# Performance work log

Measured on AMD Instinct MI355X. Metric: run time of the kernel, lower is better.

The kernel has to match this reference:

```python
import jax, jax.numpy as jnp
import numpy as np

WZ, WH, WW = 2, 6, 12            # window_size (pressure, lat, lon)
DIM, HEADS = 192, 6
N_TOK = WZ * WH * WW             # 144 tokens per window
TYPE_WIN = (14 // WZ) * (721 // WH)  # 840 window types
TABLE = (2 * WW - 1) * WH * WH * WZ * WZ  # 3312 bias rows


def _position_index():
    # Earth-specific (asymmetric in z/h) relative position index, per _construct_index
    zi = np.arange(WZ); zj = -np.arange(WZ) * WZ
    hi = np.arange(WH); hj = -np.arange(WH) * WH
    w = np.arange(WW)
    c1 = np.stack(np.meshgrid(zi, hi, w, indexing='ij')).reshape(3, -1)
    c2 = np.stack(np.meshgrid(zj, hj, w, indexing='ij')).reshape(3, -1)
    coords = (c1[:, :, None] - c2[:, None, :]).transpose(1, 2, 0)
    coords[:, :, 2] += WW - 1
    coords[:, :, 1] *= 2 * WW - 1
    coords[:, :, 0] *= (2 * WW - 1) * WH * WH
    return jnp.asarray(coords.sum(-1).reshape(-1), dtype=jnp.int32)  # (N*N,)


def setup_inputs() -> dict:
    key = jax.random.key(0)
    ks = jax.random.split(key, 8)
    B = 2
    x = jax.random.normal(ks[0], (B, TYPE_WIN, N_TOK, DIM), dtype=jnp.float32)
    mask = jax.random.normal(ks[1], (B, N_TOK, N_TOK), dtype=jnp.float32)
    w1 = jax.random.normal(ks[2], (3 * DIM, DIM), dtype=jnp.float32) * 0.02
    b1 = jnp.zeros((3 * DIM,), dtype=jnp.float32)
    w2 = jax.random.normal(ks[3], (DIM, DIM), dtype=jnp.float32) * 0.02
    b2 = jnp.zeros((DIM,), dtype=jnp.float32)
    bias_table = jax.random.normal(ks[4], (TABLE, TYPE_WIN, HEADS), dtype=jnp.float32) * 0.02
    return {"x": x, "mask": mask, "w1": w1, "b1": b1, "w2": w2, "b2": b2,
            "bias_table": bias_table, "position_index": _position_index()}


def reference(x, mask, w1, b1, w2, b2, bias_table, position_index):
    B, nW, N, C = x.shape
    d = C // HEADS
    scale = d ** (-0.5)
    qkv = (jnp.einsum('bwnc,oc->bwno', x, w1) + b1).reshape(B, nW, N, 3, HEADS, d)
    q, k, v = jnp.moveaxis(qkv, 3, 0)           # each (B, nW, N, H, d)
    attn = jnp.einsum('bwnhd,bwmhd->bwhnm', q * scale, k)  # (B, nW, H, N, N)
    # gather earth-specific bias: (N*N,) -> (N, N, nW, H) -> (nW, H, N, N)
    bias = bias_table[position_index].reshape(N, N, nW, HEADS).transpose(2, 3, 0, 1)
    attn = attn + bias[None] + mask[:, None, None, :, :]
    attn = jax.nn.softmax(attn, axis=-1)
    out = jnp.einsum('bwhnm,bwmhd->bwnhd', attn, v).reshape(B, nW, N, C)
    return jnp.einsum('bwnc,oc->bwno', out, w2) + b2
```

## Files before the change

### kernel.cpp

```cpp
#include <hip/hip_runtime.h>
#include <cstdint>
#include <cstddef>

typedef unsigned short u16;
typedef __bf16 bf16x8 __attribute__((ext_vector_type(8)));
typedef u16    u16x8  __attribute__((ext_vector_type(8)));
typedef float  f32x4  __attribute__((ext_vector_type(4)));

#define NW 840
#define NTOK 144
#define DIM 192
#define HEADS 6
#define TABLE_ROWS 3312
#define SCALE 0.17677669529663687f

__device__ __forceinline__ u16 f2b_bits(float f) {
  unsigned u = __builtin_bit_cast(unsigned, f);
  return (u16)((u + 0x7FFFu + ((u >> 16) & 1u)) >> 16);
}

__device__ __forceinline__ bf16x8 ld_bf8(const u16* p) {
  return __builtin_bit_cast(bf16x8, *(const u16x8*)p);
}

__device__ __forceinline__ f32x4 mfma16(bf16x8 a, bf16x8 b, f32x4 c) {
  return __builtin_amdgcn_mfma_f32_16x16x32_bf16(a, b, c, 0, 0, 0);
}

__global__ void k_prep(const float* __restrict__ bt, const float* __restrict__ w1,
                       const float* __restrict__ w2, float* __restrict__ bto,
                       u16* __restrict__ w1b, u16* __restrict__ w2b) {
  __shared__ float tile[64 * 65];
  int bid = blockIdx.x, tid = threadIdx.x;
  if (bid < 52 * 79) {
    int p0 = (bid % 52) * 64;
    int wh0 = (bid / 52) * 64;
    #pragma unroll
    for (int it = 0; it < 16; ++it) {
      int idx = tid + it * 256;
      int pp = idx >> 6, cc = idx & 63;
      float v = 0.f;
      if (p0 + pp < TABLE_ROWS && wh0 + cc < NW * HEADS)
        v = bt[(size_t)(p0 + pp) * (NW * HEADS) + wh0 + cc];
      tile[pp * 65 + cc] = v;
    }
    __syncthreads();
    #pragma unroll
    for (int it = 0; it < 16; ++it) {
      int idx = tid + it * 256;
      int rr = idx >> 6, cc2 = idx & 63;
      if (wh0 + rr < NW * HEADS && p0 + cc2 < TABLE_ROWS)
        bto[(size_t)(wh0 + rr) * TABLE_ROWS + p0 + cc2] = tile[cc2 * 65 + rr];
    }
  } else {
    int i = (bid - 52 * 79) * 256 + tid;
    if (i < 576 * DIM) {
      w1b[i] = f2b_bits(w1[i]);
    } else {
      int j = i - 576 * DIM;
      if (j < DIM * DIM) w2b[j] = f2b_bits(w2[j]);
    }
  }
}

__global__ __launch_bounds__(576) void k_attn(
    const float* __restrict__ x, const float* __restrict__ mask,
    const float* __restrict__ b1, const u16* __restrict__ w1b,
    const float* __restrict__ bias_t, const int* __restrict__ pos,
    u16* __restrict__ Ow) {
  __shared__ __align__(16) u16 q_lds[NTOK * 40];
  __shared__ __align__(16) u16 k_lds[NTOK * 40];
  __shared__ __align__(16) u16 vt[32 * 168];
  __shared__ __align__(16) u16 pch[NTOK * 40];
  __shared__ float bias_s[TABLE_ROWS];

  const int tid = threadIdx.x;
  const int w = tid >> 6;
  const int l = tid & 63;
  const int c = l & 15;
  const int q4 = l >> 4;
  const int bw = blockIdx.x;
  const int b = bw / NW;
  const int ww = bw % NW;

  const float* xg = x + (size_t)bw * (NTOK * DIM);

  if (tid < 512) vt[(tid >> 4) * 168 + 144 + (tid & 15)] = 0;

  const int m3 = w % 3;
  const int p = w / 3;
  const int r = w;
  bf16x8 xf[3][6];
  #pragma unroll
  for (int i = 0; i < 3; ++i) {
    const int mti = m3 + 3 * i;
    const float* rp = xg + (size_t)(mti * 16 + c) * DIM;
    #pragma unroll
    for (int ks = 0; ks < 6; ++ks) {
      const float4* fp = (const float4*)(rp + ks * 32 + q4 * 8);
      float4 f0 = fp[0], f1 = fp[1];
      u16x8 rr;
      rr[0] = f2b_bits(f0.x); rr[1] = f2b_bits(f0.y);
      rr[2] = f2b_bits(f0.z); rr[3] = f2b_bits(f0.w);
      rr[4] = f2b_bits(f1.x); rr[5] = f2b_bits(f1.y);
      rr[6] = f2b_bits(f1.z); rr[7] = f2b_bits(f1.w);
      xf[i][ks] = __builtin_bit_cast(bf16x8, rr);
    }
  }

  const f32x4 z = {0.f, 0.f, 0.f, 0.f};
  const int n0 = r * 16 + q4 * 4;
  const int* pr[4];
  const float* mr[4];
  #pragma unroll
  for (int g = 0; g < 4; ++g) {
    pr[g] = pos + (n0 + g) * NTOK;
    mr[g] = mask + (size_t)b * (NTOK * NTOK) + (size_t)(n0 + g) * NTOK;
  }

  for (int h = 0; h < HEADS; ++h) {
    f32x4 acc[3][2];
    #pragma unroll
    for (int i = 0; i < 3; ++i) { acc[i][0] = z; acc[i][1] = z; }
    const int obase = p * DIM + h * 32;
    #pragma unroll
    for (int ks = 0; ks < 6; ++ks) {
      bf16x8 w0 = ld_bf8(w1b + (size_t)(obase + c) * DIM + ks * 32 + q4 * 8);
      bf16x8 w1f = ld_bf8(w1b + (size_t)(obase + 16 + c) * DIM + ks * 32 + q4 * 8);
      #pragma unroll
      for (int i = 0; i < 3; ++i) {
        acc[i][0] = mfma16(xf[i][ks], w0, acc[i][0]);
        acc[i][1] = mfma16(xf[i][ks], w1f, acc[i][1]);
      }
    }
    float b1v[2] = {b1[obase + c], b1[obase + 16 + c]};

    if (p < 2) {
      u16* dst = (p == 0) ? q_lds : k_lds;
      #pragma unroll
      for (int i = 0; i < 3; ++i) {
        const int rowb = (m3 + 3 * i) * 16 + q4 * 4;
        #pragma unroll
        for (int j = 0; j < 2; ++j)
          #pragma unroll
          for (int reg = 0; reg < 4; ++reg)
            dst[(rowb + reg) * 40 + j * 16 + c] = f2b_bits(acc[i][j][reg] + b1v[j]);
      }
    } else {
      #pragma unroll
      for (int i = 0; i < 3; ++i) {
        const int mb = (m3 + 3 * i) * 16 + q4 * 4;
        #pragma unroll
        for (int j = 0; j < 2; ++j) {
          unsigned lo = (unsigned)f2b_bits(acc[i][j][0] + b1v[j]) |
                        ((unsigned)f2b_bits(acc[i][j][1] + b1v[j]) << 16);
          unsigned hi = (unsigned)f2b_bits(acc[i][j][2] + b1v[j]) |
                        ((unsigned)f2b_bits(acc[i][j][3] + b1v[j]) << 16);
          uint2 u; u.x = lo; u.y = hi;
          *(uint2*)&vt[(j * 16 + c) * 168 + mb] = u;
        }
      }
    }

    {
      const float* src = bias_t + (size_t)(ww * HEADS + h) * TABLE_ROWS;
      for (int idx = tid; idx < TABLE_ROWS; idx += 576) bias_s[idx] = src[idx];
    }
    __syncthreads();

    bf16x8 qa = ld_bf8(&q_lds[(r * 16 + c) * 40 + q4 * 8]);
    f32x4 S[9];
    #pragma unroll
    for (int ct = 0; ct < 9; ++ct)
      S[ct] = mfma16(qa, ld_bf8(&k_lds[(ct * 16 + c) * 40 + q4 * 8]), z);

    #pragma unroll
    for (int ct = 0; ct < 9; ++ct) {
      const int m = ct * 16 + c;
      #pragma unroll
      for (int g = 0; g < 4; ++g)
        S[ct][g] = S[ct][g] * SCALE + bias_s[pr[g][m]] + mr[g][m];
    }
    float mx[4] = {-3e38f, -3e38f, -3e38f, -3e38f};
    #pragma unroll
    for (int ct = 0; ct < 9; ++ct)
      #pragma unroll
      for (int g = 0; g < 4; ++g) mx[g] = fmaxf(mx[g], S[ct][g]);
    #pragma unroll
    for (int g = 0; g < 4; ++g) {
      mx[g] = fmaxf(mx[g], __shfl_xor(mx[g], 1));
      mx[g] = fmaxf(mx[g], __shfl_xor(mx[g], 2));
      mx[g] = fmaxf(mx[g], __shfl_xor(mx[g], 4));
      mx[g] = fmaxf(mx[g], __shfl_xor(mx[g], 8));
    }
    float sm[4] = {0.f, 0.f, 0.f, 0.f};
    #pragma unroll
    for (int ct = 0; ct < 9; ++ct)
      #pragma unroll
      for (int g = 0; g < 4; ++g) {
        float e = __expf(S[ct][g] - mx[g]);
        S[ct][g] = e;
        sm[g] += e;
      }
    #pragma unroll
    for (int g = 0; g < 4; ++g) {
      sm[g] += __shfl_xor(sm[g], 1);
      sm[g] += __shfl_xor(sm[g], 2);
      sm[g] += __shfl_xor(sm[g], 4);
      sm[g] += __shfl_xor(sm[g], 8);
    }
    float inv[4];
    #pragma unroll
    for (int g = 0; g < 4; ++g) inv[g] = 1.0f / sm[g];

    f32x4 oacc[2] = {z, z};
    #pragma unroll
    for (int ks = 0; ks < 5; ++ks) {
      #pragma unroll
      for (int cti = 0; cti < 2; ++cti) {
        const int ct = 2 * ks + cti;
        #pragma unroll
        for (int g = 0; g < 4; ++g) {
          u16 pv = 0;
          if (ct < 9) pv = f2b_bits(S[ct][g] * inv[g]);
          pch[(r * 16 + q4 * 4 + g) * 40 + cti * 16 + c] = pv;
        }
      }
      __asm__ volatile("" ::: "memory");
      bf16x8 pa = ld_bf8(&pch[(r * 16 + c) * 40 + q4 * 8]);
      oacc[0] = mfma16(pa, ld_bf8(&vt[(c) * 168 + ks * 32 + q4 * 8]), oacc[0]);
      oacc[1] = mfma16(pa, ld_bf8(&vt[(16 + c) * 168 + ks * 32 + q4 * 8]), oacc[1]);
      __asm__ volatile("" ::: "memory");
    }

    #pragma unroll
    for (int j = 0; j < 2; ++j)
      #pragma unroll
      for (int g = 0; g < 4; ++g)
        Ow[((size_t)bw * NTOK + r * 16 + q4 * 4 + g) * DIM + h * 32 + j * 16 + c] =
            f2b_bits(oacc[j][g]);

    __syncthreads();
  }
}

__global__ __launch_bounds__(576) void k_proj(const u16* __restrict__ Ow,
                                              const u16* __restrict__ w2b,
                                              const float* __restrict__ b2,
                                              float* __restrict__ out) {
  const int tid = threadIdx.x;
  const int w = tid >> 6;
  const int l = tid & 63;
  const int c = l & 15, q4 = l >> 4;
  const int bw = blockIdx.x;
  const int m3 = w % 3, ntg = w / 3;
  const size_t rbase = (size_t)bw * NTOK;

  const f32x4 z = {0.f, 0.f, 0.f, 0.f};
  f32x4 acc[3][4];
  #pragma unroll
  for (int i = 0; i < 3; ++i)
    #pragma unroll
    for (int j = 0; j < 4; ++j) acc[i][j] = z;

  #pragma unroll
  for (int ks = 0; ks < 6; ++ks) {
    bf16x8 af[3];
    #pragma unroll
    for (int i = 0; i < 3; ++i)
      af[i] = ld_bf8(Ow + (rbase + (m3 + 3 * i) * 16 + c) * DIM + ks * 32 + q4 * 8);
    bf16x8 bfg[4];
    #pragma unroll
    for (int j = 0; j < 4; ++j)
      bfg[j] = ld_bf8(w2b + (size_t)(ntg * 64 + j * 16 + c) * DIM + ks * 32 + q4 * 8);
    #pragma unroll
    for (int i = 0; i < 3; ++i)
      #pragma unroll
      for (int j = 0; j < 4; ++j) acc[i][j] = mfma16(af[i], bfg[j], acc[i][j]);
  }

  float b2v[4];
  #pragma unroll
  for (int j = 0; j < 4; ++j) b2v[j] = b2[ntg * 64 + j * 16 + c];

  #pragma unroll
  for (int i = 0; i < 3; ++i) {
    const int rowb = (m3 + 3 * i) * 16 + q4 * 4;
    #pragma unroll
    for (int j = 0; j < 4; ++j)
      #pragma unroll
      for (int g = 0; g < 4; ++g)
        out[(rbase + rowb + g) * DIM + ntg * 64 + j * 16 + c] = acc[i][j][g] + b2v[j];
  }
}

extern "C" void kernel_launch(void* const* d_in, const int* in_sizes, int n_in,
                              void* d_out, int out_size, void* d_ws, size_t ws_size,
                              hipStream_t stream) {
  const float* x = (const float*)d_in[0];
  const float* mask = (const float*)d_in[1];
  const float* w1 = (const float*)d_in[2];
  const float* b1 = (const float*)d_in[3];
  const float* w2 = (const float*)d_in[4];
  const float* b2 = (const float*)d_in[5];
  const float* bias_table = (const float*)d_in[6];
  const int* pos = (const int*)d_in[7];
  float* out = (float*)d_out;

  char* ws = (char*)d_ws;
  float* bias_t = (float*)ws;
  u16* w1b = (u16*)(ws + 66769920);
  u16* w2b = (u16*)(ws + 66991104);
  u16* Ow = (u16*)(ws + 67064832);

  k_prep<<<dim3(52 * 79 + 576), dim3(256), 0, stream>>>(bias_table, w1, w2,
                                                        bias_t, w1b, w2b);
  k_attn<<<dim3(2 * NW), dim3(576), 0, stream>>>(x, mask, b1, w1b, bias_t, pos, Ow);
  k_proj<<<dim3(2 * NW), dim3(576), 0, stream>>>(Ow, w2b, b2, out);
}
```

Baseline: 1.267 ms.

## Split attention kernel into one block per window-head with 3 waves

Restructures k_attn so each block handles a single (window, head) pair with 192 threads instead of looping over all 6 heads in a 576-thread block. Each block recomputes x-to-bf16 conversion and computes Q/K/V for its head only, removes the per-head bias table staging in LDS and per-head syncs, and reads bias and position index directly from global memory. The aim is higher occupancy and fewer barriers, at the cost of reloading and reconverting x six times per window and doing uncached gathered global reads for the bias.

Result: faster. 1.035 ms (-18.3%).

```diff
diff --git a/kernel.cpp b/kernel.cpp
--- a/kernel.cpp
+++ b/kernel.cpp
@@ -63,38 +63,45 @@
   }
 }
 
-__global__ __launch_bounds__(576) void k_attn(
+__global__ __launch_bounds__(192, 3) void k_attn(
     const float* __restrict__ x, const float* __restrict__ mask,
     const float* __restrict__ b1, const u16* __restrict__ w1b,
     const float* __restrict__ bias_t, const int* __restrict__ pos,
     u16* __restrict__ Ow) {
-  __shared__ __align__(16) u16 q_lds[NTOK * 40];
-  __shared__ __align__(16) u16 k_lds[NTOK * 40];
+  __shared__ __align__(16) u16 q_lds[NTOK * 36];
+  __shared__ __align__(16) u16 k_lds[NTOK * 36];
   __shared__ __align__(16) u16 vt[32 * 168];
-  __shared__ __align__(16) u16 pch[NTOK * 40];
-  __shared__ float bias_s[TABLE_ROWS];
+  __shared__ __align__(16) u16 pch[3 * 16 * 40];
 
   const int tid = threadIdx.x;
   const int w = tid >> 6;
   const int l = tid & 63;
   const int c = l & 15;
   const int q4 = l >> 4;
-  const int bw = blockIdx.x;
+  const int bid = blockIdx.x;
+  const int h = bid % HEADS;
+  const int bw = bid / HEADS;
   const int b = bw / NW;
   const int ww = bw % NW;
 
   const float* xg = x + (size_t)bw * (NTOK * DIM);
-
-  if (tid < 512) vt[(tid >> 4) * 168 + 144 + (tid & 15)] = 0;
-
-  const int m3 = w % 3;
-  const int p = w / 3;
-  const int r = w;
-  bf16x8 xf[3][6];
-  #pragma unroll
-  for (int i = 0; i < 3; ++i) {
-    const int mti = m3 + 3 * i;
-    const float* rp = xg + (size_t)(mti * 16 + c) * DIM;
+  const float* bias_g = bias_t + (size_t)(ww * HEADS + h) * TABLE_ROWS;
+  const float* mask_g = mask + (size_t)b * (NTOK * NTOK);
+
+  for (int i = tid; i < 512; i += 192) vt[(i >> 4) * 168 + 144 + (i & 15)] = 0;
+
+  float b1v[6];
+  #pragma unroll
+  for (int pp = 0; pp < 3; ++pp)
+    #pragma unroll
+    for (int jj = 0; jj < 2; ++jj)
+      b1v[pp * 2 + jj] = b1[pp * DIM + h * 32 + jj * 16 + c];
+
+  #pragma unroll
+  for (int mt = 0; mt < 3; ++mt) {
+    const int tile = w + 3 * mt;
+    bf16x8 af[6];
+    const float* rp = xg + (size_t)(tile * 16 + c) * DIM;
     #pragma unroll
     for (int ks = 0; ks < 6; ++ks) {
       const float4* fp = (const float4*)(rp + ks * 32 + q4 * 8);
@@ -104,82 +111,62 @@
       rr[2] = f2b_bits(f0.z); rr[3] = f2b_bits(f0.w);
       rr[4] = f2b_bits(f1.x); rr[5] = f2b_bits(f1.y);
       rr[6] = f2b_bits(f1.z); rr[7] = f2b_bits(f1.w);
-      xf[i][ks] = __builtin_bit_cast(bf16x8, rr);
-    }
-  }
-
+      af[ks] = __builtin_bit_cast(bf16x8, rr);
+    }
+    const f32x4 z = {0.f, 0.f, 0.f, 0.f};
+    f32x4 acc[6];
+    #pragma unroll
+    for (int u = 0; u < 6; ++u) acc[u] = z;
+    #pragma unroll
+    for (int ks = 0; ks < 6; ++ks) {
+      #pragma unroll
+      for (int pp = 0; pp < 3; ++pp)
+        #pragma unroll
+        for (int jj = 0; jj < 2; ++jj) {
+          bf16x8 bfr = ld_bf8(w1b + (size_t)(pp * DIM + h * 32 + jj * 16 + c) * DIM +
+                              ks * 32 + q4 * 8);
+          acc[pp * 2 + jj] = mfma16(af[ks], bfr, acc[pp * 2 + jj]);
+        }
+    }
+    #pragma unroll
+    for (int jj = 0; jj < 2; ++jj) {
+      #pragma unroll
+      for (int g = 0; g < 4; ++g) {
+        const int row = tile * 16 + q4 * 4 + g;
+        q_lds[row * 36 + jj * 16 + c] = f2b_bits(acc[0 * 2 + jj][g] + b1v[jj]);
+        k_lds[row * 36 + jj * 16 + c] = f2b_bits(acc[1 * 2 + jj][g] + b1v[2 + jj]);
+      }
+      unsigned lo = (unsigned)f2b_bits(acc[4 + jj][0] + b1v[4 + jj]) |
+                    ((unsigned)f2b_bits(acc[4 + jj][1] + b1v[4 + jj]) << 16);
+      unsigned hi = (unsigned)f2b_bits(acc[4 + jj][2] + b1v[4 + jj]) |
+                    ((unsigned)f2b_bits(acc[4 + jj][3] + b1v[4 + jj]) << 16);
+      uint2 uu; uu.x = lo; uu.y = hi;
+      *(uint2*)&vt[(jj * 16 + c) * 168 + tile * 16 + q4 * 4] = uu;
+    }
+  }
+  __syncthreads();
+
+  u16* wbuf = pch + w * (16 * 40);
   const f32x4 z = {0.f, 0.f, 0.f, 0.f};
-  const int n0 = r * 16 + q4 * 4;
-  const int* pr[4];
-  const float* mr[4];
-  #pragma unroll
-  for (int g = 0; g < 4; ++g) {
-    pr[g] = pos + (n0 + g) * NTOK;
-    mr[g] = mask + (size_t)b * (NTOK * NTOK) + (size_t)(n0 + g) * NTOK;
-  }
-
-  for (int h = 0; h < HEADS; ++h) {
-    f32x4 acc[3][2];
-    #pragma unroll
-    for (int i = 0; i < 3; ++i) { acc[i][0] = z; acc[i][1] = z; }
-    const int obase = p * DIM + h * 32;
-    #pragma unroll
-    for (int ks = 0; ks < 6; ++ks) {
-      bf16x8 w0 = ld_bf8(w1b + (size_t)(obase + c) * DIM + ks * 32 + q4 * 8);
-      bf16x8 w1f = ld_bf8(w1b + (size_t)(obase + 16 + c) * DIM + ks * 32 + q4 * 8);
-      #pragma unroll
-      for (int i = 0; i < 3; ++i) {
-        acc[i][0] = mfma16(xf[i][ks], w0, acc[i][0]);
-        acc[i][1] = mfma16(xf[i][ks], w1f, acc[i][1]);
-      }
-    }
-    float b1v[2] = {b1[obase + c], b1[obase + 16 + c]};
-
-    if (p < 2) {
-      u16* dst = (p == 0) ? q_lds : k_lds;
-      #pragma unroll
-      for (int i = 0; i < 3; ++i) {
-        const int rowb = (m3 + 3 * i) * 16 + q4 * 4;
-        #pragma unroll
-        for (int j = 0; j < 2; ++j)
-          #pragma unroll
-          for (int reg = 0; reg < 4; ++reg)
-            dst[(rowb + reg) * 40 + j * 16 + c] = f2b_bits(acc[i][j][reg] + b1v[j]);
-      }
-    } else {
-      #pragma unroll
-      for (int i = 0; i < 3; ++i) {
-        const int mb = (m3 + 3 * i) * 16 + q4 * 4;
-        #pragma unroll
-        for (int j = 0; j < 2; ++j) {
-          unsigned lo = (unsigned)f2b_bits(acc[i][j][0] + b1v[j]) |
-                        ((unsigned)f2b_bits(acc[i][j][1] + b1v[j]) << 16);
-          unsigned hi = (unsigned)f2b_bits(acc[i][j][2] + b1v[j]) |
-                        ((unsigned)f2b_bits(acc[i][j][3] + b1v[j]) << 16);
-          uint2 u; u.x = lo; u.y = hi;
-          *(uint2*)&vt[(j * 16 + c) * 168 + mb] = u;
-        }
-      }
-    }
-
-    {
-      const float* src = bias_t + (size_t)(ww * HEADS + h) * TABLE_ROWS;
-      for (int idx = tid; idx < TABLE_ROWS; idx += 576) bias_s[idx] = src[idx];
-    }
-    __syncthreads();
-
-    bf16x8 qa = ld_bf8(&q_lds[(r * 16 + c) * 40 + q4 * 8]);
+  #pragma unroll 1
+  for (int rti = 0; rti < 3; ++rti) {
+    const int rt = w + 3 * rti;
+    const int n0 = rt * 16 + q4 * 4;
+
+    bf16x8 qa = ld_bf8(&q_lds[(rt * 16 + c) * 36 + q4 * 8]);
     f32x4 S[9];
     #pragma unroll
     for (int ct = 0; ct < 9; ++ct)
-      S[ct] = mfma16(qa, ld_bf8(&k_lds[(ct * 16 + c) * 40 + q4 * 8]), z);
+      S[ct] = mfma16(qa, ld_bf8(&k_lds[(ct * 16 + c) * 36 + q4 * 8]), z);
 
     #pragma unroll
     for (int ct = 0; ct < 9; ++ct) {
       const int m = ct * 16 + c;
       #pragma unroll
-      for (int g = 0; g < 4; ++g)
-        S[ct][g] = S[ct][g] * SCALE + bias_s[pr[g][m]] + mr[g][m];
+      for (int g = 0; g < 4; ++g) {
+        const int n = n0 + g;
+        S[ct][g] = S[ct][g] * SCALE + bias_g[pos[n * NTOK + m]] + mask_g[n * NTOK + m];
+      }
     }
     float mx[4] = {-3e38f, -3e38f, -3e38f, -3e38f};
     #pragma unroll
@@ -213,34 +200,31 @@
     #pragma unroll
     for (int g = 0; g < 4; ++g) inv[g] = 1.0f / sm[g];
 
-    f32x4 oacc[2] = {z, z};
-    #pragma unroll
-    for (int ks = 0; ks < 5; ++ks) {
+    f32x4 o0 = z, o1 = z;
+    #pragma unroll
+    for (int ks5 = 0; ks5 < 5; ++ks5) {
       #pragma unroll
       for (int cti = 0; cti < 2; ++cti) {
-        const int ct = 2 * ks + cti;
+        const int ct = 2 * ks5 + cti;
         #pragma unroll
         for (int g = 0; g < 4; ++g) {
           u16 pv = 0;
           if (ct < 9) pv = f2b_bits(S[ct][g] * inv[g]);
-          pch[(r * 16 + q4 * 4 + g) * 40 + cti * 16 + c] = pv;
+          wbuf[(q4 * 4 + g) * 40 + cti * 16 + c] = pv;
         }
       }
       __asm__ volatile("" ::: "memory");
-      bf16x8 pa = ld_bf8(&pch[(r * 16 + c) * 40 + q4 * 8]);
-      oacc[0] = mfma16(pa, ld_bf8(&vt[(c) * 168 + ks * 32 + q4 * 8]), oacc[0]);
-      oacc[1] = mfma16(pa, ld_bf8(&vt[(16 + c) * 168 + ks * 32 + q4 * 8]), oacc[1]);
+      bf16x8 pa = ld_bf8(&wbuf[c * 40 + q4 * 8]);
+      o0 = mfma16(pa, ld_bf8(&vt[c * 168 + ks5 * 32 + q4 * 8]), o0);
+      o1 = mfma16(pa, ld_bf8(&vt[(16 + c) * 168 + ks5 * 32 + q4 * 8]), o1);
       __asm__ volatile("" ::: "memory");
     }
 
     #pragma unroll
-    for (int j = 0; j < 2; ++j)
-      #pragma unroll
-      for (int g = 0; g < 4; ++g)
-        Ow[((size_t)bw * NTOK + r * 16 + q4 * 4 + g) * DIM + h * 32 + j * 16 + c] =
-            f2b_bits(oacc[j][g]);
-
-    __syncthreads();
+    for (int g = 0; g < 4; ++g) {
+      Ow[((size_t)bw * NTOK + n0 + g) * DIM + h * 32 + c] = f2b_bits(o0[g]);
+      Ow[((size_t)bw * NTOK + n0 + g) * DIM + h * 32 + 16 + c] = f2b_bits(o1[g]);
+    }
   }
 }
 
@@ -315,6 +299,7 @@
 
   k_prep<<<dim3(52 * 79 + 576), dim3(256), 0, stream>>>(bias_table, w1, w2,
                                                         bias_t, w1b, w2b);
-  k_attn<<<dim3(2 * NW), dim3(576), 0, stream>>>(x, mask, b1, w1b, bias_t, pos, Ow);
+  k_attn<<<dim3(2 * NW * HEADS), dim3(192), 0, stream>>>(x, mask, b1, w1b, bias_t,
+                                                         pos, Ow);
   k_proj<<<dim3(2 * NW), dim3(576), 0, stream>>>(Ow, w2b, b2, out);
 }
```
